# Optimization experiments

Hardware: AMD Instinct MI355X
Metric: run time of the kernel (lower is better)

The kernel has to match this reference:

```python
import jax, jax.numpy as jnp
import numpy as np

EMBED = 512
HEADS = 8
HD = EMBED // HEADS  # 64
NCLS = 1
WSIZE = 32
DIL = 2
WIN_LEN = 2 * WSIZE + 1  # 65


def setup_inputs() -> dict:
    key = jax.random.key(0)
    ks = jax.random.split(key, 5)
    B, S = 2, NCLS + 2048
    return {
        "x": jax.random.normal(ks[0], (B, S, EMBED), dtype=jnp.float32),
        "qkv_w": jax.random.normal(ks[1], (3 * EMBED, EMBED), dtype=jnp.float32) * 0.02,
        "qkv_b": jax.random.normal(ks[2], (3 * EMBED,), dtype=jnp.float32) * 0.02,
        "out_w": jax.random.normal(ks[3], (EMBED, EMBED), dtype=jnp.float32) * 0.02,
        "out_b": jax.random.normal(ks[4], (EMBED,), dtype=jnp.float32) * 0.02,
    }


def reference(x, qkv_w, qkv_b, out_w, out_b):
    B, S, E = x.shape
    P = S - NCLS  # patch_len
    scale = HD ** -0.5

    qkv = (x @ qkv_w.T + qkv_b).reshape(B, S, 3, HEADS, HD)
    qkv = qkv.transpose(2, 0, 3, 1, 4)  # (3, B, H, S, d)
    q, k, v = qkv[0], qkv[1], qkv[2]

    q_cls, k_cls, v_cls = q[:, :, :NCLS], k[:, :, :NCLS], v[:, :, :NCLS]
    q_p, k_p, v_p = q[:, :, NCLS:], k[:, :, NCLS:], v[:, :, NCLS:]

    # CLS queries: full attention over all S keys
    s_cls = jnp.einsum('bhqd,bhkd->bhqk', q_cls, k) * scale
    cls_out = jnp.einsum('bhqk,bhkd->bhqd', jax.nn.softmax(s_cls, axis=-1), v)

    # Patch queries: CLS keys + dilated local window
    pad = WSIZE * DIL
    kp = jnp.pad(k_p, ((0, 0), (0, 0), (pad, pad), (0, 0)))
    vp = jnp.pad(v_p, ((0, 0), (0, 0), (pad, pad), (0, 0)))
    idx = jnp.arange(P)[:, None] + jnp.arange(WIN_LEN)[None, :] * DIL  # (P, WL)
    kw = kp[:, :, idx]  # (B, H, P, WL, d)
    vw = vp[:, :, idx]

    sw = jnp.einsum('bhpd,bhpwd->bhpw', q_p, kw) * scale
    pos = jnp.arange(P)[:, None] + (jnp.arange(WIN_LEN) - WSIZE)[None, :] * DIL
    in_bounds = (pos >= 0) & (pos < P)  # (P, WL)
    sw = jnp.where(in_bounds[None, None], sw, -jnp.inf)
    sc = jnp.einsum('bhpd,bhcd->bhpc', q_p, k_cls) * scale

    attn = jax.nn.softmax(jnp.concatenate([sc, sw], axis=-1), axis=-1)
    a_c, a_w = attn[..., :NCLS], attn[..., NCLS:]
    patch_out = (jnp.einsum('bhpc,bhcd->bhpd', a_c, v_cls)
                 + jnp.einsum('bhpw,bhpwd->bhpd', a_w, vw))

    out = jnp.concatenate([cls_out, patch_out], axis=2)  # (B, H, S, d)
    out = out.transpose(0, 2, 1, 3).reshape(B, S, E)
    return out @ out_w.T + out_b
```

## Files before the change

### kernel.cpp

```cpp
#include <hip/hip_runtime.h>
#include <math.h>

#define S_LEN 2049
#define P_LEN 2048
#define EMB 512
#define NH 8
#define HD 64
#define SCALE 0.125f

typedef _Float16 f16x8 __attribute__((ext_vector_type(8)));
typedef float f32x4 __attribute__((ext_vector_type(4)));
typedef unsigned short u16x8 __attribute__((ext_vector_type(8)));

__device__ inline unsigned short f2h(float f) {
  _Float16 h = (_Float16)f;
  return __builtin_bit_cast(unsigned short, h);
}
__device__ inline float h2f(unsigned short u) {
  return (float)__builtin_bit_cast(_Float16, u);
}

__device__ inline void gld16(const unsigned* g, unsigned* l) {
  __builtin_amdgcn_global_load_lds(
      (const __attribute__((address_space(1))) unsigned*)g,
      (__attribute__((address_space(3))) unsigned*)l, 16, 0, 0);
}

__global__ __launch_bounds__(256) void cvt3_f16(
    const float* __restrict__ s0, unsigned short* __restrict__ d0, int n0,
    const float* __restrict__ s1, unsigned short* __restrict__ d1, int n1,
    const float* __restrict__ s2, unsigned short* __restrict__ d2, int n2) {
  int idx = (blockIdx.x * 256 + threadIdx.x) * 8;
  const float* s;
  unsigned short* d;
  int off;
  if (idx < n0) {
    s = s0; d = d0; off = idx;
  } else if (idx < n0 + n1) {
    s = s1; d = d1; off = idx - n0;
  } else if (idx < n0 + n1 + n2) {
    s = s2; d = d2; off = idx - n0 - n1;
  } else {
    return;
  }
  float4 f0 = *(const float4*)(s + off);
  float4 f1 = *(const float4*)(s + off + 4);
  float ff[8] = {f0.x, f0.y, f0.z, f0.w, f1.x, f1.y, f1.z, f1.w};
  u16x8 vh;
#pragma unroll
  for (int e = 0; e < 8; e++) vh[e] = f2h(ff[e]);
  *(u16x8*)(d + off) = vh;
}

template <int BM, int BN, bool F16OUT>
__global__ __launch_bounds__(256) void gemm_f16(
    const unsigned short* __restrict__ A, const unsigned short* __restrict__ B,
    const float* __restrict__ bias, void* __restrict__ Cv, int M, int N,
    int KP) {
  constexpr int BK = 64;
  __shared__ __align__(16) unsigned short As[BM * BK];
  __shared__ __align__(16) unsigned short Bs[BN * BK];
  const int t = threadIdx.x;
  const int lane = t & 63, wv = t >> 6;
  const int m0 = blockIdx.x * BM, n0 = blockIdx.y * BN;
  constexpr int WM = BM / 2, WN = BN / 2;
  constexpr int RM = WM / 16, RN = WN / 16;
  const int wm = wv & 1, wn = wv >> 1;
  const int lm = lane & 15, lq = lane >> 4;

  f32x4 acc[RM][RN];
#pragma unroll
  for (int i = 0; i < RM; i++)
#pragma unroll
    for (int j = 0; j < RN; j++) acc[i][j] = (f32x4){0.f, 0.f, 0.f, 0.f};

  const int lr = lane >> 3;
  const int lc = (lane & 7) ^ lr;

  const unsigned* aptr[BM / 32];
#pragma unroll
  for (int p = 0; p < BM / 32; p++) {
    int ra = wv * (BM / 4) + p * 8 + lr;
    int gr = m0 + ra;
    gr = gr < M ? gr : M - 1;
    aptr[p] = (const unsigned*)(A + (size_t)gr * KP + lc * 8);
  }
  const unsigned* bptr[BN / 32];
#pragma unroll
  for (int p = 0; p < BN / 32; p++) {
    int rb = wv * (BN / 4) + p * 8 + lr;
    bptr[p] = (const unsigned*)(B + (size_t)(n0 + rb) * KP + lc * 8);
  }

  for (int kt = 0; kt < KP; kt += BK) {
    __syncthreads();
#pragma unroll
    for (int p = 0; p < BM / 32; p++)
      gld16(aptr[p] + (kt >> 1), (unsigned*)&As[(wv * (BM / 4) + p * 8) * BK]);
#pragma unroll
    for (int p = 0; p < BN / 32; p++)
      gld16(bptr[p] + (kt >> 1), (unsigned*)&Bs[(wv * (BN / 4) + p * 8) * BK]);
    __syncthreads();

    f16x8 fa[2][RM], fb[2][RN];
#pragma unroll
    for (int kk = 0; kk < 2; kk++) {
      int ch = ((kk * 4 + lq) ^ (lm & 7)) * 8;
#pragma unroll
      for (int mi = 0; mi < RM; mi++) {
        int ra = wm * WM + mi * 16 + lm;
        fa[kk][mi] = *(const f16x8*)&As[ra * BK + ch];
      }
#pragma unroll
      for (int ni = 0; ni < RN; ni++) {
        int rb = wn * WN + ni * 16 + lm;
        fb[kk][ni] = *(const f16x8*)&Bs[rb * BK + ch];
      }
    }
#pragma unroll
    for (int kk = 0; kk < 2; kk++)
#pragma unroll
      for (int mi = 0; mi < RM; mi++)
#pragma unroll
        for (int ni = 0; ni < RN; ni++)
          acc[mi][ni] = __builtin_amdgcn_mfma_f32_16x16x32_f16(
              fa[kk][mi], fb[kk][ni], acc[mi][ni], 0, 0, 0);
  }

#pragma unroll
  for (int ni = 0; ni < RN; ni++) {
    int n = n0 + wn * WN + ni * 16 + lm;
    float bv = bias[n];
#pragma unroll
    for (int mi = 0; mi < RM; mi++)
#pragma unroll
      for (int r = 0; r < 4; r++) {
        int m = m0 + wm * WM + mi * 16 + lq * 4 + r;
        if (m < M) {
          float val = acc[mi][ni][r] + bv;
          if constexpr (F16OUT)
            ((unsigned short*)Cv)[(size_t)m * N + n] = f2h(val);
          else
            ((float*)Cv)[(size_t)m * N + n] = val;
        }
      }
  }
}

__global__ __launch_bounds__(256) void patch_attn3(
    const unsigned short* __restrict__ qkv16,
    unsigned short* __restrict__ Aatt) {
  constexpr int LDK = 72;
  constexpr int LDT = 168;
  __shared__ __align__(16) unsigned short Ks[144 * LDK];
  __shared__ __align__(16) unsigned short Vt[64 * LDT];
  __shared__ __align__(16) unsigned short Ps[64 * LDT];

  const int t = threadIdx.x;
  const int lane = t & 63, wv = t >> 6;
  const int lm = lane & 15, lq = lane >> 4;
  const int qb = blockIdx.x;
  const int h = blockIdx.y;
  const int par = blockIdx.z & 1, b = blockIdx.z >> 1;
  const unsigned short* base = qkv16 + (size_t)b * S_LEN * 1536;

  if (qb == 0) {
    if (par == 1) return;
    const int kidx = lane >> 3, c = lane & 7, d0 = c * 8;
    float qv[8];
    {
      f16x8 qh = *(const f16x8*)(base + h * 64 + d0);
#pragma unroll
      for (int i = 0; i < 8; i++) qv[i] = (float)qh[i] * SCALE;
    }
    float m = -1e30f, l = 0.f, o[8];
#pragma unroll
    for (int i = 0; i < 8; i++) o[i] = 0.f;

    for (int it = 0; it < 65; it++) {
      int j = it * 32 + wv * 8 + kidx;
      bool valid = j < S_LEN;
      f16x8 kh, vh;
      if (valid) {
        const unsigned short* row = base + (size_t)j * 1536 + 512 + h * 64;
        kh = *(const f16x8*)(row + d0);
        vh = *(const f16x8*)(row + 512 + d0);
      }
      float dp = 0.f;
      if (valid) {
#pragma unroll
        for (int i = 0; i < 8; i++) dp += qv[i] * (float)kh[i];
      }
#pragma unroll
      for (int off = 1; off < 8; off <<= 1) dp += __shfl_xor(dp, off, 64);
      float s = valid ? dp : -1e30f;
      float cmax = s;
#pragma unroll
      for (int off = 8; off < 64; off <<= 1)
        cmax = fmaxf(cmax, __shfl_xor(cmax, off, 64));
      float mn = fmaxf(m, cmax);
      float sc = __expf(m - mn);
      float e = valid ? __expf(s - mn) : 0.f;
      float esum = e;
#pragma unroll
      for (int off = 8; off < 64; off <<= 1) esum += __shfl_xor(esum, off, 64);
      l = l * sc + esum;
#pragma unroll
      for (int i = 0; i < 8; i++)
        o[i] = o[i] * sc + (valid ? e * (float)vh[i] : 0.f);
      m = mn;
    }
#pragma unroll
    for (int i = 0; i < 8; i++) {
#pragma unroll
      for (int off = 8; off < 64; off <<= 1) o[i] += __shfl_xor(o[i], off, 64);
    }
    float* SF = (float*)Ks;
    if (kidx == 0) {
#pragma unroll
      for (int i = 0; i < 8; i++) SF[wv * 64 + d0 + i] = o[i];
    }
    if (lane == 0) {
      SF[256 + wv] = m;
      SF[260 + wv] = l;
    }
    __syncthreads();
    if (t < 64) {
      float M = -1e30f;
#pragma unroll
      for (int i = 0; i < 4; i++) M = fmaxf(M, SF[256 + i]);
      float L = 0.f, O = 0.f;
#pragma unroll
      for (int i = 0; i < 4; i++) {
        float cexp = __expf(SF[256 + i] - M);
        L += SF[260 + i] * cexp;
        O += SF[i * 64 + t] * cexp;
      }
      Aatt[(size_t)b * S_LEN * 512 + h * HD + t] = f2h(O / L);
    }
    return;
  }

  const int qc0 = (qb - 1) * 64;

  {
    uint4 z = {0, 0, 0, 0};
    if (t < 120) {
      int r = 129 + (t >> 3), c = (t & 7) * 8;
      *(uint4*)&Ks[r * LDK + c] = z;
    }
    {
      int r = t >> 2, c = 128 + (t & 3) * 8;
      *(uint4*)&Vt[r * LDT + c] = z;
    }
    if (t < 128) {
      int r = t >> 1, c = 144 + (t & 1) * 8;
      *(uint4*)&Ps[r * LDT + c] = z;
    }
  }
  __syncthreads();

  {
    int rr = t >> 4;
    int cc = (t & 15) * 4;
#pragma unroll
    for (int pass = 0; pass < 8; pass++) {
      int r = pass * 16 + rr;
      int jc = qc0 - 32 + r;
      uint2 kv = {0, 0};
      if ((unsigned)jc < 1024u)
        kv = *(const uint2*)(base + (size_t)(1 + 2 * jc + par) * 1536 + 512 +
                             h * 64 + cc);
      *(uint2*)&Ks[r * LDK + cc] = kv;
    }
    if (rr == 0)
      *(uint2*)&Ks[128 * LDK + cc] =
          *(const uint2*)(base + 512 + h * 64 + cc);
  }
#pragma unroll
  for (int pass = 0; pass < 4; pass++) {
    int task = pass * 256 + t;
    int jp = task >> 4;
    int d0 = (task & 15) * 4;
    int jc0 = qc0 - 32 + 2 * jp;
    uint2 a = {0, 0}, c = {0, 0};
    if ((unsigned)jc0 < 1024u)
      a = *(const uint2*)(base + (size_t)(1 + 2 * jc0 + par) * 1536 + 1024 +
                          h * 64 + d0);
    if ((unsigned)(jc0 + 1) < 1024u)
      c = *(const uint2*)(base + (size_t)(1 + 2 * (jc0 + 1) + par) * 1536 +
                          1024 + h * 64 + d0);
    *(unsigned*)&Vt[(d0 + 0) * LDT + 2 * jp] = (a.x & 0xffffu) | (c.x << 16);
    *(unsigned*)&Vt[(d0 + 1) * LDT + 2 * jp] = (a.x >> 16) | (c.x & 0xffff0000u);
    *(unsigned*)&Vt[(d0 + 2) * LDT + 2 * jp] = (a.y & 0xffffu) | (c.y << 16);
    *(unsigned*)&Vt[(d0 + 3) * LDT + 2 * jp] = (a.y >> 16) | (c.y & 0xffff0000u);
  }
  if (t < 64) Vt[t * LDT + 128] = base[1024 + h * 64 + t];

  const int qi = wv * 16 + lm;
  const unsigned short* qg =
      base + (size_t)(1 + 2 * (qc0 + qi) + par) * 1536 + h * 64;
  f16x8 qf[2];
  qf[0] = *(const f16x8*)&qg[lq * 8];
  qf[1] = *(const f16x8*)&qg[32 + lq * 8];
  __syncthreads();

  f32x4 s[9];
#pragma unroll
  for (int nt = 0; nt < 9; nt++) s[nt] = (f32x4){0.f, 0.f, 0.f, 0.f};
#pragma unroll
  for (int nt = 0; nt < 9; nt++) {
#pragma unroll
    for (int kk = 0; kk < 2; kk++) {
      f16x8 kb = *(const f16x8*)&Ks[(nt * 16 + lm) * LDK + kk * 32 + lq * 8];
      s[nt] =
          __builtin_amdgcn_mfma_f32_16x16x32_f16(qf[kk], kb, s[nt], 0, 0, 0);
    }
  }

  float L[4];
#pragma unroll
  for (int r = 0; r < 4; r++) {
    int qrow = wv * 16 + lq * 4 + r;
    float sv[9];
    float mx = -1e30f;
#pragma unroll
    for (int nt = 0; nt < 9; nt++) {
      int jl = nt * 16 + lm;
      bool valid =
          (jl == 128) ||
          (jl < 128 && jl >= qrow && jl <= qrow + 64 &&
           (unsigned)(qc0 - 32 + jl) < 1024u);
      sv[nt] = valid ? s[nt][r] * SCALE : -1e30f;
      mx = fmaxf(mx, sv[nt]);
    }
#pragma unroll
    for (int off = 1; off < 16; off <<= 1)
      mx = fmaxf(mx, __shfl_xor(mx, off, 16));
    float l = 0.f;
#pragma unroll
    for (int nt = 0; nt < 9; nt++) {
      float e = __expf(sv[nt] - mx);
      l += e;
      Ps[qrow * LDT + nt * 16 + lm] = f2h(e);
    }
#pragma unroll
    for (int off = 1; off < 16; off <<= 1) l += __shfl_xor(l, off, 16);
    L[r] = l;
  }
  __syncthreads();

  f32x4 oa[4];
#pragma unroll
  for (int nt = 0; nt < 4; nt++) oa[nt] = (f32x4){0.f, 0.f, 0.f, 0.f};
#pragma unroll
  for (int kc = 0; kc < 5; kc++) {
    f16x8 pa = *(const f16x8*)&Ps[(wv * 16 + lm) * LDT + kc * 32 + lq * 8];
#pragma unroll
    for (int nt = 0; nt < 4; nt++) {
      f16x8 vb = *(const f16x8*)&Vt[(nt * 16 + lm) * LDT + kc * 32 + lq * 8];
      oa[nt] = __builtin_amdgcn_mfma_f32_16x16x32_f16(pa, vb, oa[nt], 0, 0, 0);
    }
  }

#pragma unroll
  for (int r = 0; r < 4; r++) {
    float inv = 1.f / L[r];
    int qrow = wv * 16 + lq * 4 + r;
    int pp = 2 * (qc0 + qrow) + par;
    unsigned short* ab = Aatt + ((size_t)b * S_LEN + 1 + pp) * 512 + h * 64;
#pragma unroll
    for (int nt = 0; nt < 4; nt++) ab[nt * 16 + lm] = f2h(oa[nt][r] * inv);
  }
}

extern "C" void kernel_launch(void* const* d_in, const int* in_sizes, int n_in,
                              void* d_out, int out_size, void* d_ws,
                              size_t ws_size, hipStream_t stream) {
  const float* x = (const float*)d_in[0];
  const float* qkv_w = (const float*)d_in[1];
  const float* qkv_b = (const float*)d_in[2];
  const float* out_w = (const float*)d_in[3];
  const float* out_b = (const float*)d_in[4];
  float* out = (float*)d_out;

  const int M = 2 * S_LEN;

  unsigned short* Xp = (unsigned short*)((float*)d_ws + 33792);
  unsigned short* Wq = Xp + (size_t)M * 512;
  unsigned short* Wo = Wq + (size_t)1536 * 512;
  unsigned short* Aatt = Wo + (size_t)512 * 512;
  unsigned short* qkv16 = Aatt + (size_t)M * 512;

  const int n0 = M * EMB;
  const int n1 = 1536 * EMB;
  const int n2 = EMB * EMB;
  int cvt_blocks = ((n0 + n1 + n2) / 8 + 255) / 256;
  cvt3_f16<<<cvt_blocks, 256, 0, stream>>>(x, Xp, n0, qkv_w, Wq, n1, out_w, Wo,
                                           n2);

  dim3 gq((M + 63) / 64, 1536 / 128);
  gemm_f16<64, 128, true><<<gq, 256, 0, stream>>>(Xp, Wq, qkv_b, qkv16, M,
                                                  1536, 512);

  patch_attn3<<<dim3(17, NH, 4), 256, 0, stream>>>(qkv16, Aatt);

  dim3 go((M + 63) / 64, EMB / 64);
  gemm_f16<64, 64, false><<<go, 256, 0, stream>>>(Aatt, Wo, out_b, out, M, EMB,
                                                  512);
}
```

Measured before the change: 143.4 us.

## Split CLS attention across two blocks and merge partials in out-proj prologue

The CLS query's full attention over all keys is now divided between two blocks (par 0 and 1), which were previously idle or returned early. Each lane keeps its own online-softmax state, and lanes are merged once at the end rather than doing cross-lane max and sum reductions on every key step. Each block writes partial max, sum and output vectors to workspace. The output-projection GEMM blocks covering the CLS rows combine these partials and write the CLS attention row before loading A. This shortens the serial tail of the CLS block, at the cost of extra workspace traffic and a small prologue with a vmcnt wait in the GEMM.

Measured after the change: 122.4 us. -14.7%, faster.

```diff
diff --git a/kernel.cpp b/kernel.cpp
--- a/kernel.cpp
+++ b/kernel.cpp
@@ -52,11 +52,12 @@
   *(u16x8*)(d + off) = vh;
 }
 
-template <int BM, int BN, bool F16OUT>
+template <int BM, int BN, bool F16OUT, bool CLSFIX>
 __global__ __launch_bounds__(256) void gemm_f16(
     const unsigned short* __restrict__ A, const unsigned short* __restrict__ B,
     const float* __restrict__ bias, void* __restrict__ Cv, int M, int N,
-    int KP) {
+    int KP, unsigned short* __restrict__ Afix, const float* __restrict__ Pm,
+    const float* __restrict__ Pl, const float* __restrict__ Po) {
   constexpr int BK = 64;
   __shared__ __align__(16) unsigned short As[BM * BK];
   __shared__ __align__(16) unsigned short Bs[BN * BK];
@@ -68,6 +69,24 @@
   const int wm = wv & 1, wn = wv >> 1;
   const int lm = lane & 15, lq = lane >> 4;
 
+  if constexpr (CLSFIX) {
+    if ((m0 == 0 || m0 == 2048) && t < 64) {
+      int bb = (m0 == 0) ? 0 : 1;
+      unsigned short* dst = Afix + (size_t)(bb * S_LEN) * 512;
+#pragma unroll
+      for (int hh = 0; hh < NH; hh++) {
+        int i0 = (bb * NH + hh) * 2;
+        float pm0 = Pm[i0], pm1 = Pm[i0 + 1];
+        float Mx = fmaxf(pm0, pm1);
+        float e0 = __expf(pm0 - Mx), e1 = __expf(pm1 - Mx);
+        float L = Pl[i0] * e0 + Pl[i0 + 1] * e1;
+        float O = Po[(size_t)i0 * 64 + t] * e0 + Po[(size_t)(i0 + 1) * 64 + t] * e1;
+        dst[hh * 64 + t] = f2h(O / L);
+      }
+    }
+    asm volatile("s_waitcnt vmcnt(0)" ::: "memory");
+  }
+
   f32x4 acc[RM][RN];
 #pragma unroll
   for (int i = 0; i < RM; i++)
@@ -148,8 +167,8 @@
 }
 
 __global__ __launch_bounds__(256) void patch_attn3(
-    const unsigned short* __restrict__ qkv16,
-    unsigned short* __restrict__ Aatt) {
+    const unsigned short* __restrict__ qkv16, unsigned short* __restrict__ Aatt,
+    float* __restrict__ Pm, float* __restrict__ Pl, float* __restrict__ Po) {
   constexpr int LDK = 72;
   constexpr int LDT = 168;
   __shared__ __align__(16) unsigned short Ks[144 * LDK];
@@ -165,8 +184,10 @@
   const unsigned short* base = qkv16 + (size_t)b * S_LEN * 1536;
 
   if (qb == 0) {
-    if (par == 1) return;
     const int kidx = lane >> 3, c = lane & 7, d0 = c * 8;
+    const int st = wv * 8 + kidx;
+    const int jbase = par * 1025;
+    const int count = par ? 1024 : 1025;
     float qv[8];
     {
       f16x8 qh = *(const f16x8*)(base + h * 64 + d0);
@@ -176,44 +197,44 @@
     float m = -1e30f, l = 0.f, o[8];
 #pragma unroll
     for (int i = 0; i < 8; i++) o[i] = 0.f;
-
-    for (int it = 0; it < 65; it++) {
-      int j = it * 32 + wv * 8 + kidx;
-      bool valid = j < S_LEN;
-      f16x8 kh, vh;
+    for (int it = 0; it < 33; it++) {
+      int rel = it * 32 + st;
+      bool valid = rel < count;
+      float dp = 0.f;
+      f16x8 vh;
       if (valid) {
-        const unsigned short* row = base + (size_t)j * 1536 + 512 + h * 64;
-        kh = *(const f16x8*)(row + d0);
+        const unsigned short* row =
+            base + (size_t)(jbase + rel) * 1536 + 512 + h * 64;
+        f16x8 kh = *(const f16x8*)(row + d0);
         vh = *(const f16x8*)(row + 512 + d0);
-      }
-      float dp = 0.f;
-      if (valid) {
 #pragma unroll
         for (int i = 0; i < 8; i++) dp += qv[i] * (float)kh[i];
       }
 #pragma unroll
       for (int off = 1; off < 8; off <<= 1) dp += __shfl_xor(dp, off, 64);
-      float s = valid ? dp : -1e30f;
-      float cmax = s;
-#pragma unroll
-      for (int off = 8; off < 64; off <<= 1)
-        cmax = fmaxf(cmax, __shfl_xor(cmax, off, 64));
-      float mn = fmaxf(m, cmax);
+      float sv = valid ? dp : -1e30f;
+      float mn = fmaxf(m, sv);
       float sc = __expf(m - mn);
-      float e = valid ? __expf(s - mn) : 0.f;
-      float esum = e;
-#pragma unroll
-      for (int off = 8; off < 64; off <<= 1) esum += __shfl_xor(esum, off, 64);
-      l = l * sc + esum;
+      float e = valid ? __expf(sv - mn) : 0.f;
+      l = l * sc + e;
 #pragma unroll
       for (int i = 0; i < 8; i++)
         o[i] = o[i] * sc + (valid ? e * (float)vh[i] : 0.f);
       m = mn;
     }
 #pragma unroll
-    for (int i = 0; i < 8; i++) {
-#pragma unroll
-      for (int off = 8; off < 64; off <<= 1) o[i] += __shfl_xor(o[i], off, 64);
+    for (int off = 8; off < 64; off <<= 1) {
+      float m2 = __shfl_xor(m, off, 64);
+      float l2 = __shfl_xor(l, off, 64);
+      float mn = fmaxf(m, m2);
+      float e0 = __expf(m - mn), e1 = __expf(m2 - mn);
+      l = l * e0 + l2 * e1;
+#pragma unroll
+      for (int i = 0; i < 8; i++) {
+        float o2 = __shfl_xor(o[i], off, 64);
+        o[i] = o[i] * e0 + o2 * e1;
+      }
+      m = mn;
     }
     float* SF = (float*)Ks;
     if (kidx == 0) {
@@ -226,17 +247,22 @@
     }
     __syncthreads();
     if (t < 64) {
-      float M = -1e30f;
-#pragma unroll
-      for (int i = 0; i < 4; i++) M = fmaxf(M, SF[256 + i]);
+      float Mx = -1e30f;
+#pragma unroll
+      for (int i = 0; i < 4; i++) Mx = fmaxf(Mx, SF[256 + i]);
       float L = 0.f, O = 0.f;
 #pragma unroll
       for (int i = 0; i < 4; i++) {
-        float cexp = __expf(SF[256 + i] - M);
-        L += SF[260 + i] * cexp;
-        O += SF[i * 64 + t] * cexp;
-      }
-      Aatt[(size_t)b * S_LEN * 512 + h * HD + t] = f2h(O / L);
+        float ce = __expf(SF[256 + i] - Mx);
+        L += SF[260 + i] * ce;
+        O += SF[i * 64 + t] * ce;
+      }
+      int idx = (b * NH + h) * 2 + par;
+      if (t == 0) {
+        Pm[idx] = Mx;
+        Pl[idx] = L;
+      }
+      Po[(size_t)idx * 64 + t] = O;
     }
     return;
   }
@@ -386,7 +412,10 @@
 
   const int M = 2 * S_LEN;
 
-  unsigned short* Xp = (unsigned short*)((float*)d_ws + 33792);
+  float* cls_pm = (float*)d_ws;
+  float* cls_pl = cls_pm + 512;
+  float* cls_po = cls_pl + 512;
+  unsigned short* Xp = (unsigned short*)(cls_po + 32768);
   unsigned short* Wq = Xp + (size_t)M * 512;
   unsigned short* Wo = Wq + (size_t)1536 * 512;
   unsigned short* Aatt = Wo + (size_t)512 * 512;
@@ -400,12 +429,13 @@
                                            n2);
 
   dim3 gq((M + 63) / 64, 1536 / 128);
-  gemm_f16<64, 128, true><<<gq, 256, 0, stream>>>(Xp, Wq, qkv_b, qkv16, M,
-                                                  1536, 512);
-
-  patch_attn3<<<dim3(17, NH, 4), 256, 0, stream>>>(qkv16, Aatt);
+  gemm_f16<64, 128, true, false><<<gq, 256, 0, stream>>>(
+      Xp, Wq, qkv_b, qkv16, M, 1536, 512, nullptr, nullptr, nullptr, nullptr);
+
+  patch_attn3<<<dim3(17, NH, 4), 256, 0, stream>>>(qkv16, Aatt, cls_pm, cls_pl,
+                                                   cls_po);
 
   dim3 go((M + 63) / 64, EMB / 64);
-  gemm_f16<64, 64, false><<<go, 256, 0, stream>>>(Aatt, Wo, out_b, out, M, EMB,
-                                                  512);
-}
+  gemm_f16<64, 64, false, true><<<go, 256, 0, stream>>>(
+      Aatt, Wo, out_b, out, M, EMB, 512, Aatt, cls_pm, cls_pl, cls_po);
+}
```
